# Kernel optimization log

Measured on AMD Instinct MI355X. Metric: run time of the kernel, lower is better.

## Reference

```python
import jax, jax.numpy as jnp
import numpy as np

C = 19
IGNORE = 255
UPPER_BOUND = 1.0
SEG_W, EDGE_W, ATT_W = 1.0, 0.3, 0.1
EDGE_THRESH = 0.8


def _img_hist(t):
    # torch.histc(target, bins=C, min=0, max=C): bin i counts values in [i, i+1); 255 falls outside
    tf = t.ravel()
    inb = (tf >= 0) & (tf < C)
    idx = jnp.where(inb, tf, 0)
    return jnp.zeros((C,), jnp.float32).at[idx].add(inb.astype(jnp.float32))


def _seg_loss(segin, target):
    # per-image class-histogram weights (ImageBasedCrossEntropyLoss2d, norm=False)
    N = target.shape[0]
    bins = jax.vmap(_img_hist)(target)                      # [N, C]
    hist_norm = bins / jnp.sum(bins, axis=1, keepdims=True)
    w = (bins != 0).astype(jnp.float32) * UPPER_BOUND * (1.0 - hist_norm) + 1.0  # [N, C]

    logp = jax.nn.log_softmax(segin, axis=1)                # [N, C, H, W]
    tc = jnp.clip(target, 0, C - 1)
    lp = jnp.take_along_axis(logp, tc[:, None, :, :], axis=1)[:, 0]  # [N, H, W]
    valid = (target != IGNORE).astype(jnp.float32)
    pw = jnp.take_along_axis(w, tc.reshape(N, -1), axis=1).reshape(target.shape) * valid
    # NLLLoss(weight, reduction='mean', ignore_index): weighted mean per image, summed over batch
    num = -jnp.sum(pw * lp, axis=(1, 2))
    den = jnp.sum(pw, axis=(1, 2))
    return jnp.sum(num / den)


def _bce2d(x, t):
    # x: logits [N,1,H,W]; t: float target, 1=pos, 0=neg, >1 ignored (weight 0)
    pos = t == 1.0
    neg = t == 0.0
    pos_num = jnp.sum(pos.astype(jnp.float32))
    neg_num = jnp.sum(neg.astype(jnp.float32))
    sum_num = pos_num + neg_num
    w = jnp.where(pos, neg_num / sum_num, 0.0) + jnp.where(neg, pos_num / sum_num, 0.0)
    # stable BCE-with-logits
    bce = jnp.maximum(x, 0.0) - x * t + jnp.log1p(jnp.exp(-jnp.abs(x)))
    return jnp.mean(w * bce)


def setup_inputs() -> dict:
    key = jax.random.key(0)
    k1, k2, k3, k4 = jax.random.split(key, 4)
    N, H, W = 4, 768, 768
    segin = jax.random.normal(k1, (N, C, H, W), dtype=jnp.float32)
    edgein = jax.random.normal(k2, (N, 1, H, W), dtype=jnp.float32)
    segmask = jax.random.randint(k3, (N, H, W), 0, C, dtype=jnp.int32)
    edgemask = jax.random.randint(k4, (N, 1, H, W), 0, 2, dtype=jnp.int32)
    return {"segin": segin, "edgein": edgein, "segmask": segmask, "edgemask": edgemask}


def reference(segin, edgein, segmask, edgemask):
    seg_loss = SEG_W * _seg_loss(segin, segmask)
    edge_loss = EDGE_W * _bce2d(edgein, edgemask.astype(jnp.float32))
    # edge attention: pixels where max-channel edge logit > 0.8 keep their label, else ignore
    edge_max = jnp.max(edgein, axis=1)                      # [N, H, W]
    att_target = jnp.where(edge_max > EDGE_THRESH, segmask, IGNORE)
    att_loss = ATT_W * _seg_loss(segin, att_target)
    return seg_loss + edge_loss + att_loss
```

## Files before the change

### kernel.cpp

```cpp
#include <hip/hip_runtime.h>
#include <math.h>

#define CNUM 19
#define NB 4
#define HW 589824
#define NPIX 2359296

#define TPB 256
#define PXT 4
#define TILE (TPB * PXT)

typedef float f32x4 __attribute__((ext_vector_type(4)));

struct ImgAcc2 {
  double sS[CNUM];
  double sA[CNUM];
  unsigned int cS[CNUM];
  unsigned int cA[CNUM];
  unsigned int pad[2];
};

struct Ws {
  ImgAcc2 img[NB];
  double bce_p, bce_n;
  unsigned int np, nn;
};

__global__ void k_init(Ws* ws) {
  unsigned int* p = (unsigned int*)ws;
  const int nw = (int)(sizeof(Ws) / 4);
  for (int i = threadIdx.x; i < nw; i += blockDim.x) p[i] = 0u;
}

__global__ __launch_bounds__(TPB, 4) void k_fused(const float* __restrict__ segin,
                                                  const float* __restrict__ edgein,
                                                  const int* __restrict__ segmask,
                                                  const int* __restrict__ edgemask,
                                                  Ws* __restrict__ wsw) {
  const int n = blockIdx.y;
  const int t = threadIdx.x;
  const int tile0 = blockIdx.x * TILE;

  __shared__ float lsS[CNUM], lsA[CNUM];
  __shared__ unsigned int lcS[CNUM], lcA[CNUM];
  __shared__ float sbp, sbn;
  __shared__ unsigned int snp, snn;

  if (t < CNUM) { lsS[t] = 0.f; lsA[t] = 0.f; lcS[t] = 0u; lcA[t] = 0u; }
  if (t == CNUM)     { sbp = 0.f; sbn = 0.f; }
  if (t == CNUM + 1) { snp = 0u;  snn = 0u; }
  __syncthreads();

  const int pxoff = n * HW + tile0 + t * 4;

  int4 tm = *reinterpret_cast<const int4*>(segmask + pxoff);
  int tcv[PXT];
  unsigned int inbits = 0u;
  {
    int ta[4] = {tm.x, tm.y, tm.z, tm.w};
    #pragma unroll
    for (int j = 0; j < 4; ++j) {
      tcv[j] = min(max(ta[j], 0), CNUM - 1);
      inbits |= (((unsigned)ta[j]) < (unsigned)CNUM) ? (1u << j) : 0u;
    }
  }

  float sacc[PXT] = {0.f, 0.f, 0.f, 0.f};
  float xt[PXT]   = {0.f, 0.f, 0.f, 0.f};

  const float* cb = segin + (size_t)n * CNUM * HW + tile0 + t * 4;
  #pragma unroll
  for (int c = 0; c < CNUM; ++c) {
    f32x4 v = __builtin_nontemporal_load(
        reinterpret_cast<const f32x4*>(cb + (size_t)c * HW));
    float va[4] = {v.x, v.y, v.z, v.w};
    #pragma unroll
    for (int j = 0; j < 4; ++j) {
      sacc[j] += __expf(va[j]);
      xt[j] = (tcv[j] == c) ? va[j] : xt[j];
    }
  }

  f32x4 ev = __builtin_nontemporal_load(reinterpret_cast<const f32x4*>(edgein + pxoff));
  int4   em = *reinterpret_cast<const int4*>(edgemask + pxoff);

  float bpos = 0.f, bneg = 0.f;
  int cntp = 0, cntn = 0;
  {
    float ea[4] = {ev.x, ev.y, ev.z, ev.w};
    int   ma[4] = {em.x, em.y, em.z, em.w};
    #pragma unroll
    for (int j = 0; j < PXT; ++j) {
      float nlp = __logf(sacc[j]) - xt[j];
      if ((inbits >> j) & 1u) {
        atomicAdd(&lsS[tcv[j]], nlp);
        atomicAdd(&lcS[tcv[j]], 1u);
        if (ea[j] > 0.8f) {
          atomicAdd(&lsA[tcv[j]], nlp);
          atomicAdd(&lcA[tcv[j]], 1u);
        }
      }
      float e = ea[j];
      int m = ma[j];
      float bce = fmaxf(e, 0.f) - e * (float)m + log1pf(__expf(-fabsf(e)));
      if (m == 1) { bpos += bce; ++cntp; }
      else if (m == 0) { bneg += bce; ++cntn; }
    }
  }

  #pragma unroll
  for (int off = 32; off > 0; off >>= 1) {
    bpos += __shfl_down(bpos, off);
    bneg += __shfl_down(bneg, off);
    cntp += __shfl_down(cntp, off);
    cntn += __shfl_down(cntn, off);
  }
  if ((t & 63) == 0) {
    atomicAdd(&sbp, bpos);
    atomicAdd(&sbn, bneg);
    atomicAdd(&snp, (unsigned int)cntp);
    atomicAdd(&snn, (unsigned int)cntn);
  }
  __syncthreads();

  if (t < CNUM) {
    atomicAdd(&wsw->img[n].sS[t], (double)lsS[t]);
  } else if (t >= 32 && t < 32 + CNUM) {
    atomicAdd(&wsw->img[n].sA[t - 32], (double)lsA[t - 32]);
  } else if (t >= 64 && t < 64 + CNUM) {
    unsigned int v = lcS[t - 64];
    if (v) atomicAdd(&wsw->img[n].cS[t - 64], v);
  } else if (t >= 96 && t < 96 + CNUM) {
    unsigned int v = lcA[t - 96];
    if (v) atomicAdd(&wsw->img[n].cA[t - 96], v);
  } else if (t == 128) {
    atomicAdd(&wsw->bce_p, (double)sbp);
  } else if (t == 129) {
    atomicAdd(&wsw->bce_n, (double)sbn);
  } else if (t == 130) {
    atomicAdd(&wsw->np, snp);
  } else if (t == 131) {
    atomicAdd(&wsw->nn, snn);
  }
}

__global__ void k_final(const Ws* __restrict__ ws, float* __restrict__ out) {
  if (threadIdx.x == 0 && blockIdx.x == 0) {
    double segl = 0.0, attl = 0.0;
    for (int i = 0; i < NB; ++i) {
      const ImgAcc2* a = &ws->img[i];
      double totS = 0.0, totA = 0.0;
      for (int c = 0; c < CNUM; ++c) { totS += (double)a->cS[c]; totA += (double)a->cA[c]; }
      double numS = 0.0, denS = 0.0, numA = 0.0, denA = 0.0;
      for (int c = 0; c < CNUM; ++c) {
        double bS = (double)a->cS[c];
        double wS = (bS != 0.0 ? (1.0 - bS / totS) : 0.0) + 1.0;
        numS += wS * a->sS[c];
        denS += wS * bS;
        double bA = (double)a->cA[c];
        double wA = (bA != 0.0 ? (1.0 - bA / totA) : 0.0) + 1.0;
        numA += wA * a->sA[c];
        denA += wA * bA;
      }
      segl += numS / denS;
      attl += numA / denA;
    }
    double s = (double)ws->np + (double)ws->nn;
    double wpos = (double)ws->nn / s;
    double wneg = (double)ws->np / s;
    double edgel = (wpos * ws->bce_p + wneg * ws->bce_n) / (double)NPIX;
    out[0] = (float)(segl + 0.3 * edgel + 0.1 * attl);
  }
}

extern "C" void kernel_launch(void* const* d_in, const int* in_sizes, int n_in,
                              void* d_out, int out_size, void* d_ws, size_t ws_size,
                              hipStream_t stream) {
  const float* segin   = (const float*)d_in[0];
  const float* edgein  = (const float*)d_in[1];
  const int*   segmask = (const int*)d_in[2];
  const int*   edgemask= (const int*)d_in[3];
  Ws* ws = (Ws*)d_ws;
  float* out = (float*)d_out;

  hipLaunchKernelGGL(k_init,  dim3(1),             dim3(256), 0, stream, ws);
  hipLaunchKernelGGL(k_fused, dim3(HW / TILE, NB), dim3(TPB), 0, stream, segin, edgein, segmask, edgemask, ws);
  hipLaunchKernelGGL(k_final, dim3(1),             dim3(1),   0, stream, ws, out);
}
```

Measured before the change: 353.7 us.

## Process eight pixels per thread with per-wave LDS histograms and plain loads

Doubles per-thread work to two float4 groups per channel, which halves the grid and the number of global double atomics per image. Shared-memory class accumulators are split per wavefront to reduce LDS atomic contention, then summed before the global flush. Nontemporal loads are replaced by ordinary loads and the occupancy hint in launch bounds is dropped. The cost is higher register pressure and possibly lower occupancy.

```diff
diff --git a/kernel.cpp b/kernel.cpp
--- a/kernel.cpp
+++ b/kernel.cpp
@@ -7,10 +7,9 @@
 #define NPIX 2359296
 
 #define TPB 256
-#define PXT 4
+#define PXT 8
 #define TILE (TPB * PXT)
-
-typedef float f32x4 __attribute__((ext_vector_type(4)));
+#define G1 1024
 
 struct ImgAcc2 {
   double sS[CNUM];
@@ -32,72 +31,81 @@
   for (int i = threadIdx.x; i < nw; i += blockDim.x) p[i] = 0u;
 }
 
-__global__ __launch_bounds__(TPB, 4) void k_fused(const float* __restrict__ segin,
-                                                  const float* __restrict__ edgein,
-                                                  const int* __restrict__ segmask,
-                                                  const int* __restrict__ edgemask,
-                                                  Ws* __restrict__ wsw) {
+__global__ __launch_bounds__(TPB) void k_fused(const float* __restrict__ segin,
+                                               const float* __restrict__ edgein,
+                                               const int* __restrict__ segmask,
+                                               const int* __restrict__ edgemask,
+                                               Ws* __restrict__ wsw) {
   const int n = blockIdx.y;
   const int t = threadIdx.x;
   const int tile0 = blockIdx.x * TILE;
 
-  __shared__ float lsS[CNUM], lsA[CNUM];
-  __shared__ unsigned int lcS[CNUM], lcA[CNUM];
+  __shared__ float lsS[4][CNUM + 1], lsA[4][CNUM + 1];
+  __shared__ unsigned int lcS[4][CNUM + 1], lcA[4][CNUM + 1];
   __shared__ float sbp, sbn;
   __shared__ unsigned int snp, snn;
 
-  if (t < CNUM) { lsS[t] = 0.f; lsA[t] = 0.f; lcS[t] = 0u; lcA[t] = 0u; }
-  if (t == CNUM)     { sbp = 0.f; sbn = 0.f; }
-  if (t == CNUM + 1) { snp = 0u;  snn = 0u; }
+  if (t < 4 * (CNUM + 1)) {
+    ((float*)lsS)[t] = 0.f; ((float*)lsA)[t] = 0.f;
+    ((unsigned int*)lcS)[t] = 0u; ((unsigned int*)lcA)[t] = 0u;
+  }
+  if (t == 128) { sbp = 0.f; sbn = 0.f; snp = 0u; snn = 0u; }
   __syncthreads();
 
-  const int pxoff = n * HW + tile0 + t * 4;
-
-  int4 tm = *reinterpret_cast<const int4*>(segmask + pxoff);
+  const int px0 = n * HW + tile0 + t * 4;
+  const int px1 = px0 + G1;
+
+  int4 tm0 = *reinterpret_cast<const int4*>(segmask + px0);
+  int4 tm1 = *reinterpret_cast<const int4*>(segmask + px1);
   int tcv[PXT];
   unsigned int inbits = 0u;
   {
-    int ta[4] = {tm.x, tm.y, tm.z, tm.w};
+    int ta[PXT] = {tm0.x, tm0.y, tm0.z, tm0.w, tm1.x, tm1.y, tm1.z, tm1.w};
     #pragma unroll
-    for (int j = 0; j < 4; ++j) {
+    for (int j = 0; j < PXT; ++j) {
       tcv[j] = min(max(ta[j], 0), CNUM - 1);
       inbits |= (((unsigned)ta[j]) < (unsigned)CNUM) ? (1u << j) : 0u;
     }
   }
 
-  float sacc[PXT] = {0.f, 0.f, 0.f, 0.f};
-  float xt[PXT]   = {0.f, 0.f, 0.f, 0.f};
+  float sacc[PXT], xt[PXT];
+  #pragma unroll
+  for (int j = 0; j < PXT; ++j) { sacc[j] = 0.f; xt[j] = 0.f; }
 
   const float* cb = segin + (size_t)n * CNUM * HW + tile0 + t * 4;
   #pragma unroll
   for (int c = 0; c < CNUM; ++c) {
-    f32x4 v = __builtin_nontemporal_load(
-        reinterpret_cast<const f32x4*>(cb + (size_t)c * HW));
-    float va[4] = {v.x, v.y, v.z, v.w};
+    const float* p = cb + (size_t)c * HW;
+    float4 v0 = *reinterpret_cast<const float4*>(p);
+    float4 v1 = *reinterpret_cast<const float4*>(p + G1);
+    float va[PXT] = {v0.x, v0.y, v0.z, v0.w, v1.x, v1.y, v1.z, v1.w};
     #pragma unroll
-    for (int j = 0; j < 4; ++j) {
+    for (int j = 0; j < PXT; ++j) {
       sacc[j] += __expf(va[j]);
       xt[j] = (tcv[j] == c) ? va[j] : xt[j];
     }
   }
 
-  f32x4 ev = __builtin_nontemporal_load(reinterpret_cast<const f32x4*>(edgein + pxoff));
-  int4   em = *reinterpret_cast<const int4*>(edgemask + pxoff);
-
+  float4 e0 = *reinterpret_cast<const float4*>(edgein + px0);
+  float4 e1 = *reinterpret_cast<const float4*>(edgein + px1);
+  int4   m0 = *reinterpret_cast<const int4*>(edgemask + px0);
+  int4   m1 = *reinterpret_cast<const int4*>(edgemask + px1);
+
+  const int wv = t >> 6;
   float bpos = 0.f, bneg = 0.f;
   int cntp = 0, cntn = 0;
   {
-    float ea[4] = {ev.x, ev.y, ev.z, ev.w};
-    int   ma[4] = {em.x, em.y, em.z, em.w};
+    float ea[PXT] = {e0.x, e0.y, e0.z, e0.w, e1.x, e1.y, e1.z, e1.w};
+    int   ma[PXT] = {m0.x, m0.y, m0.z, m0.w, m1.x, m1.y, m1.z, m1.w};
     #pragma unroll
     for (int j = 0; j < PXT; ++j) {
       float nlp = __logf(sacc[j]) - xt[j];
       if ((inbits >> j) & 1u) {
-        atomicAdd(&lsS[tcv[j]], nlp);
-        atomicAdd(&lcS[tcv[j]], 1u);
+        atomicAdd(&lsS[wv][tcv[j]], nlp);
+        atomicAdd(&lcS[wv][tcv[j]], 1u);
         if (ea[j] > 0.8f) {
-          atomicAdd(&lsA[tcv[j]], nlp);
-          atomicAdd(&lcA[tcv[j]], 1u);
+          atomicAdd(&lsA[wv][tcv[j]], nlp);
+          atomicAdd(&lcA[wv][tcv[j]], 1u);
         }
       }
       float e = ea[j];
@@ -124,15 +132,20 @@
   __syncthreads();
 
   if (t < CNUM) {
-    atomicAdd(&wsw->img[n].sS[t], (double)lsS[t]);
+    float v = lsS[0][t] + lsS[1][t] + lsS[2][t] + lsS[3][t];
+    atomicAdd(&wsw->img[n].sS[t], (double)v);
   } else if (t >= 32 && t < 32 + CNUM) {
-    atomicAdd(&wsw->img[n].sA[t - 32], (double)lsA[t - 32]);
+    int c = t - 32;
+    float v = lsA[0][c] + lsA[1][c] + lsA[2][c] + lsA[3][c];
+    atomicAdd(&wsw->img[n].sA[c], (double)v);
   } else if (t >= 64 && t < 64 + CNUM) {
-    unsigned int v = lcS[t - 64];
-    if (v) atomicAdd(&wsw->img[n].cS[t - 64], v);
+    int c = t - 64;
+    unsigned int v = lcS[0][c] + lcS[1][c] + lcS[2][c] + lcS[3][c];
+    if (v) atomicAdd(&wsw->img[n].cS[c], v);
   } else if (t >= 96 && t < 96 + CNUM) {
-    unsigned int v = lcA[t - 96];
-    if (v) atomicAdd(&wsw->img[n].cA[t - 96], v);
+    int c = t - 96;
+    unsigned int v = lcA[0][c] + lcA[1][c] + lcA[2][c] + lcA[3][c];
+    if (v) atomicAdd(&wsw->img[n].cA[c], v);
   } else if (t == 128) {
     atomicAdd(&wsw->bce_p, (double)sbp);
   } else if (t == 129) {
```

New measurement: 301.6 us. 1.17x faster.
